# Performance work log

Hardware: AMD Instinct MI355X
Metric: run time of the kernel (lower is better)

Reference implementation:

```python
import jax, jax.numpy as jnp
import numpy as np

B, M, S, D, Q, H = 8, 8192, 128, 512, 32, 8
HD = D // H
LN_EPS = 1e-5


def setup_inputs() -> dict:
    key = jax.random.key(0)
    ks = jax.random.split(key, 12)
    inp = {
        "memory": jax.random.normal(ks[0], (B, M, D), dtype=jnp.float32),
        "context": jax.random.normal(ks[1], (B, S, D), dtype=jnp.float32),
        "memory_mask": jax.random.randint(ks[2], (B, M), 0, 2).astype(bool),
        # learned parameters
        "queries_param": jax.random.normal(ks[3], (Q, D), dtype=jnp.float32) * 0.02,
        "ctx_w": jax.random.normal(ks[4], (D, D), dtype=jnp.float32) / np.sqrt(D),
        "ctx_b": jnp.zeros((D,), dtype=jnp.float32),
        "in_w": jax.random.normal(ks[5], (3 * D, D), dtype=jnp.float32) / np.sqrt(D),
        "in_b": jnp.zeros((3 * D,), dtype=jnp.float32),
        "out_w": jax.random.normal(ks[6], (D, D), dtype=jnp.float32) / np.sqrt(D),
        "out_b": jnp.zeros((D,), dtype=jnp.float32),
        "ln_g": jnp.ones((D,), dtype=jnp.float32),
        "ln_b": jnp.zeros((D,), dtype=jnp.float32),
        "gate_w": jax.random.normal(ks[7], (Q, D), dtype=jnp.float32) / np.sqrt(D),
        "gate_b": jnp.zeros((Q,), dtype=jnp.float32),
    }
    return inp


def _forward(memory, context, memory_mask, queries_param, ctx_w, ctx_b,
             in_w, in_b, out_w, out_b, ln_g, ln_b, gate_w, gate_b):
    b = memory.shape[0]
    # pool context over sequence dim (rank-3 path)
    pooled = context.mean(axis=1)  # [B, D]
    # queries + projected context
    queries = queries_param[None, :, :] + (pooled @ ctx_w.T + ctx_b)[:, None, :]  # [B, Q, D]
    # MultiheadAttention in-projection
    wq, wk, wv = in_w[:D], in_w[D:2 * D], in_w[2 * D:]
    bq, bk, bv = in_b[:D], in_b[D:2 * D], in_b[2 * D:]
    qh = (queries @ wq.T + bq).reshape(b, Q, H, HD).transpose(0, 2, 1, 3)   # [B,H,Q,hd]
    kh = (memory @ wk.T + bk).reshape(b, M, H, HD).transpose(0, 2, 1, 3)    # [B,H,M,hd]
    vh = (memory @ wv.T + bv).reshape(b, M, H, HD).transpose(0, 2, 1, 3)    # [B,H,M,hd]
    scale = 1.0 / np.sqrt(HD)
    scores = jnp.einsum('bhqd,bhkd->bhqk', qh * scale, kh)                  # [B,H,Q,M]
    # key_padding_mask: True in memory_mask means valid; invalid -> -inf
    scores = jnp.where(memory_mask[:, None, None, :], scores, -jnp.inf)
    attn = jax.nn.softmax(scores, axis=-1)                                   # [B,H,Q,M]
    ctx_out = jnp.einsum('bhqk,bhkd->bhqd', attn, vh)
    ctx_out = ctx_out.transpose(0, 2, 1, 3).reshape(b, Q, D)
    readouts = ctx_out @ out_w.T + out_b                                     # [B,Q,D]
    attention = attn.mean(axis=1)                                            # [B,Q,M]
    gates = jax.nn.sigmoid(pooled @ gate_w.T + gate_b)                       # [B,Q]
    readouts = readouts * gates[:, :, None]
    mu = readouts.mean(axis=-1, keepdims=True)
    var = readouts.var(axis=-1, keepdims=True)
    readouts_norm = (readouts - mu) * jax.lax.rsqrt(var + LN_EPS) * ln_g + ln_b
    return readouts_norm, attention, gates, queries


def reference(memory, context, memory_mask, queries_param, ctx_w, ctx_b,
              in_w, in_b, out_w, out_b, ln_g, ln_b, gate_w, gate_b):
    return _forward(memory, context, memory_mask, queries_param, ctx_w, ctx_b,
                    in_w, in_b, out_w, out_b, ln_g, ln_b, gate_w, gate_b)
```

## Files before the change

### kernel.cpp

```cpp
#include <hip/hip_runtime.h>
#include <cstdint>

#define BB 8
#define MM 8192
#define SS 128
#define DD 512
#define QQ 32
#define HH 8
#define HDD 64
#define LN_EPS 1e-5f

typedef __bf16 bf16;
typedef __attribute__((ext_vector_type(8))) __bf16 bf16x8;
typedef __attribute__((ext_vector_type(4))) __bf16 bf16x4;
typedef __attribute__((ext_vector_type(4))) float f32x4;

__global__ __launch_bounds__(512) void k_front(const float* __restrict__ ctx,
                                               const float* __restrict__ ctx_w,
                                               const float* __restrict__ ctx_b,
                                               const float* __restrict__ qp,
                                               const float* __restrict__ gate_w,
                                               const float* __restrict__ gate_b,
                                               float* __restrict__ q_out,
                                               float* __restrict__ gates_out) {
    __shared__ float pl[DD];
    int b = blockIdx.x, t = threadIdx.x;
    const float* p = ctx + (size_t)b * SS * DD + t;
    float s = 0.f;
#pragma unroll 8
    for (int i = 0; i < SS; i++) s += p[(size_t)i * DD];
    pl[t] = s * (1.0f / SS);
    __syncthreads();
    const f32x4* wr = (const f32x4*)(ctx_w + (size_t)t * DD);
    const f32x4* pv = (const f32x4*)pl;
    float acc = 0.f;
#pragma unroll 8
    for (int k = 0; k < DD / 4; k++) {
        f32x4 w = wr[k], pp = pv[k];
        acc += w.x * pp.x + w.y * pp.y + w.z * pp.z + w.w * pp.w;
    }
    float proj = acc + ctx_b[t];
#pragma unroll 4
    for (int q = 0; q < QQ; q++)
        q_out[((size_t)b * QQ + q) * DD + t] = qp[q * DD + t] + proj;
    if (t < QQ) {
        const f32x4* gw = (const f32x4*)(gate_w + (size_t)t * DD);
        float ga = 0.f;
#pragma unroll 8
        for (int k = 0; k < DD / 4; k++) {
            f32x4 w = gw[k], pp = pv[k];
            ga += w.x * pp.x + w.y * pp.y + w.z * pp.z + w.w * pp.w;
        }
        gates_out[b * QQ + t] = 1.0f / (1.0f + __expf(-(ga + gate_b[t])));
    }
}

__global__ void k_qh(const float* __restrict__ q_in, const float* __restrict__ in_w,
                     const float* __restrict__ in_b, float* __restrict__ qh) {
    __shared__ float qr[DD];
    int bq = blockIdx.x, t = threadIdx.x;
    qr[t] = q_in[(size_t)bq * DD + t];
    qr[t + 256] = q_in[(size_t)bq * DD + t + 256];
    __syncthreads();
    const f32x4* qv = (const f32x4*)qr;
#pragma unroll
    for (int jj = 0; jj < 2; jj++) {
        int j = t + jj * 256;
        const f32x4* wv = (const f32x4*)(in_w + (size_t)j * DD);
        float acc = 0.f;
#pragma unroll 8
        for (int k = 0; k < DD / 4; k++) {
            f32x4 w = wv[k], p = qv[k];
            acc += w.x * p.x + w.y * p.y + w.z * p.z + w.w * p.w;
        }
        qh[(size_t)bq * DD + j] = 0.125f * (acc + in_b[j]);
    }
}

__global__ void k_cvt(const float* __restrict__ src, bf16* __restrict__ dst, int n4) {
    int i = blockIdx.x * blockDim.x + threadIdx.x;
    if (i >= n4) return;
    f32x4 v = ((const f32x4*)src)[i];
    bf16x4 o;
    o.x = (bf16)v.x; o.y = (bf16)v.y; o.z = (bf16)v.z; o.w = (bf16)v.w;
    ((bf16x4*)dst)[i] = o;
}

__global__ __launch_bounds__(512) void k_gemm_kv(const bf16* __restrict__ A,
                                                 const bf16* __restrict__ Bw,
                                                 const float* __restrict__ in_b,
                                                 bf16* __restrict__ kvK,
                                                 bf16* __restrict__ Vt) {
    __shared__ __align__(16) bf16 sm[2 * 128 * 64];
    bf16* As = sm;
    bf16* Bs = sm + 128 * 64;
    int tid = threadIdx.x;
    int w = tid >> 6, l = tid & 63;
    int bid = blockIdx.x;
    int bn = (bid >> 3) & 7;
    int bm = ((bid >> 6) << 3) | (bid & 7);
    int wm = w >> 1, wn = w & 1;
    const f32x4 vzero = {0.f, 0.f, 0.f, 0.f};
    f32x4 acc[2][4];
#pragma unroll
    for (int i = 0; i < 2; i++)
#pragma unroll
        for (int j = 0; j < 4; j++) acc[i][j] = vzero;

    int lr = l >> 3;
    int gc = (l & 7) ^ lr;
    const bf16* Ag = A + (size_t)(bm * 128) * DD;
    const bf16* Bg = Bw + (size_t)(bn * 128) * DD;
    int lq = l & 15, quad = l >> 4, lx = lq & 7;

    for (int k0 = 0; k0 < DD; k0 += 64) {
        __syncthreads();
#pragma unroll
        for (int i = 0; i < 2; i++) {
            int seg = w * 2 + i;
            const bf16* ga = Ag + (size_t)(seg * 8 + lr) * DD + k0 + gc * 8;
            const bf16* gb = Bg + (size_t)(seg * 8 + lr) * DD + k0 + gc * 8;
            __builtin_amdgcn_global_load_lds((const __attribute__((address_space(1))) void*)ga,
                                             (__attribute__((address_space(3))) void*)(As + seg * 512),
                                             16, 0, 0);
            __builtin_amdgcn_global_load_lds((const __attribute__((address_space(1))) void*)gb,
                                             (__attribute__((address_space(3))) void*)(Bs + seg * 512),
                                             16, 0, 0);
        }
        __syncthreads();
#pragma unroll
        for (int kc = 0; kc < 8; kc += 4) {
            int ch = (quad + kc) ^ lx;
            bf16x8 af[2], bfr[4];
#pragma unroll
            for (int i = 0; i < 2; i++)
                af[i] = *(const bf16x8*)(As + (wm * 32 + i * 16 + lq) * 64 + ch * 8);
#pragma unroll
            for (int j = 0; j < 4; j++)
                bfr[j] = *(const bf16x8*)(Bs + (wn * 64 + j * 16 + lq) * 64 + ch * 8);
#pragma unroll
            for (int i = 0; i < 2; i++)
#pragma unroll
                for (int j = 0; j < 4; j++)
                    acc[i][j] = __builtin_amdgcn_mfma_f32_16x16x32_bf16(af[i], bfr[j], acc[i][j], 0, 0, 0);
        }
    }

    __syncthreads();
    bf16* tile = sm;
    if (bn < 4) {
#pragma unroll
        for (int j = 0; j < 4; j++) {
            int col = wn * 64 + j * 16 + lq;
            float bias = in_b[512 + bn * 128 + col];
            int cc = col >> 3, cl = col & 7;
#pragma unroll
            for (int i = 0; i < 2; i++) {
                int rbase = wm * 32 + i * 16 + quad * 4;
#pragma unroll
                for (int t = 0; t < 4; t++) {
                    int row = rbase + t;
                    tile[row * 128 + ((cc ^ (row & 15)) << 3) + cl] = (bf16)(acc[i][j][t] + bias);
                }
            }
        }
        __syncthreads();
        for (int idx = tid; idx < 2048; idx += 512) {
            int row = idx >> 4, ch2 = idx & 15;
            bf16x8 v = *(const bf16x8*)(tile + row * 128 + ((ch2 ^ (row & 15)) << 3));
            *(bf16x8*)(kvK + (size_t)(bm * 128 + row) * 512 + bn * 128 + ch2 * 8) = v;
        }
    } else {
#pragma unroll
        for (int j = 0; j < 4; j++) {
            int col = wn * 64 + j * 16 + lq;
            float bias = in_b[512 + bn * 128 + col];
            int cs = col & 15;
#pragma unroll
            for (int i = 0; i < 2; i++) {
                int rbase = wm * 32 + i * 16 + quad * 4;
#pragma unroll
                for (int t = 0; t < 4; t++) {
                    int row = rbase + t;
                    tile[col * 128 + (((row >> 3) ^ cs) << 3) + (row & 7)] = (bf16)(acc[i][j][t] + bias);
                }
            }
        }
        __syncthreads();
        int b = bm >> 6;
        int m0 = (bm & 63) * 128;
        int hd0 = (bn - 4) * 128;
        for (int idx = tid; idx < 2048; idx += 512) {
            int col = idx >> 4, ch2 = idx & 15;
            bf16x8 v = *(const bf16x8*)(tile + col * 128 + ((ch2 ^ (col & 15)) << 3));
            *(bf16x8*)(Vt + ((size_t)(b * 512 + hd0 + col)) * MM + m0 + ch2 * 8) = v;
        }
    }
}

__global__ __launch_bounds__(256) void k_scores(const float* __restrict__ qh,
                                                const bf16* __restrict__ kvK,
                                                const int* __restrict__ mask,
                                                float* __restrict__ scores) {
    int blk = blockIdx.x;
    int mt = blk & 15, h = (blk >> 4) & 7, b = blk >> 7;
    int tid = threadIdx.x, w = tid >> 6, l = tid & 63;
    int lq = l & 15, quad = l >> 4;
    int mbase = mt * 512 + w * 128;

    bf16x8 af[2][2];
#pragma unroll
    for (int i = 0; i < 2; i++)
#pragma unroll
        for (int s = 0; s < 2; s++) {
            const float* qp = qh + ((size_t)(b * QQ + i * 16 + lq)) * DD + h * 64 + s * 32 + quad * 8;
            f32x4 q0 = *(const f32x4*)qp;
            f32x4 q1 = *(const f32x4*)(qp + 4);
            bf16x8 v;
            v[0] = (bf16)q0.x; v[1] = (bf16)q0.y; v[2] = (bf16)q0.z; v[3] = (bf16)q0.w;
            v[4] = (bf16)q1.x; v[5] = (bf16)q1.y; v[6] = (bf16)q1.z; v[7] = (bf16)q1.w;
            af[i][s] = v;
        }

    const f32x4 vzero = {0.f, 0.f, 0.f, 0.f};
    f32x4 acc[2][8];
#pragma unroll
    for (int i = 0; i < 2; i++)
#pragma unroll
        for (int n = 0; n < 8; n++) acc[i][n] = vzero;

#pragma unroll
    for (int n = 0; n < 8; n++) {
        int m = mbase + n * 16 + lq;
        const bf16* kp = kvK + ((size_t)(b * MM + m)) * 512 + h * 64 + quad * 8;
        bf16x8 b0 = *(const bf16x8*)kp;
        bf16x8 b1 = *(const bf16x8*)(kp + 32);
#pragma unroll
        for (int i = 0; i < 2; i++) {
            acc[i][n] = __builtin_amdgcn_mfma_f32_16x16x32_bf16(af[i][0], b0, acc[i][n], 0, 0, 0);
            acc[i][n] = __builtin_amdgcn_mfma_f32_16x16x32_bf16(af[i][1], b1, acc[i][n], 0, 0, 0);
        }
    }
#pragma unroll
    for (int n = 0; n < 8; n++) {
        int m = mbase + n * 16 + lq;
        int mv = mask[b * MM + m];
        float ninf = -__builtin_inff();
#pragma unroll
        for (int i = 0; i < 2; i++)
#pragma unroll
            for (int t = 0; t < 4; t++) {
                int q = i * 16 + quad * 4 + t;
                float val = mv ? acc[i][n][t] : ninf;
                scores[((size_t)(b * HH + h) * QQ + q) * MM + m] = val;
            }
    }
}

__global__ __launch_bounds__(1024) void k_softmax(float* __restrict__ scores,
                                                  float* __restrict__ attn_out) {
    __shared__ float sred[16];
    int bq = blockIdx.x;
    int b = bq >> 5, q = bq & 31;
    int t = threadIdx.x, wid = t >> 6;
    float am[8];
#pragma unroll
    for (int i = 0; i < 8; i++) am[i] = 0.f;

    for (int h = 0; h < HH; h++) {
        float* row = scores + ((size_t)(b * HH + h) * QQ + q) * MM;
        bf16* prow = (bf16*)row;
        float x[8];
#pragma unroll
        for (int i = 0; i < 8; i++) x[i] = row[t + i * 1024];
        float mx = -__builtin_inff();
#pragma unroll
        for (int i = 0; i < 8; i++) mx = fmaxf(mx, x[i]);
        for (int off = 32; off; off >>= 1) mx = fmaxf(mx, __shfl_xor(mx, off, 64));
        if ((t & 63) == 0) sred[wid] = mx;
        __syncthreads();
#pragma unroll
        for (int i = 0; i < 16; i++) mx = fmaxf(mx, sred[i]);
        __syncthreads();
        float sum = 0.f;
#pragma unroll
        for (int i = 0; i < 8; i++) {
            x[i] = __expf(x[i] - mx);
            sum += x[i];
        }
        for (int off = 32; off; off >>= 1) sum += __shfl_xor(sum, off, 64);
        if ((t & 63) == 0) sred[wid] = sum;
        __syncthreads();
        float tot = 0.f;
#pragma unroll
        for (int i = 0; i < 16; i++) tot += sred[i];
        float inv = 1.0f / tot;
#pragma unroll
        for (int i = 0; i < 8; i++) {
            float p = x[i] * inv;
            prow[t + i * 1024] = (bf16)p;
            am[i] += p;
        }
        __syncthreads();
    }
    float* ao = attn_out + (size_t)bq * MM;
#pragma unroll
    for (int i = 0; i < 8; i++) ao[t + i * 1024] = am[i] * (1.0f / HH);
}

__global__ __launch_bounds__(256) void k_pv(const bf16* __restrict__ Pb,
                                            const bf16* __restrict__ Vt,
                                            float* __restrict__ ctxo_p) {
    __shared__ float ctile[QQ * HDD];
    int blk = blockIdx.x;
    int ck = blk & 7, h = (blk >> 3) & 7, b = blk >> 6;
    int t = threadIdx.x, w = t >> 6, l = t & 63;
    int lq = l & 15, quad = l >> 4;
    int m0 = ck * 1024 + w * 256;

    const bf16* Prow0 = Pb + ((size_t)((b * HH + h) * QQ + lq)) * 16384 + m0 + quad * 8;
    const bf16* Prow1 = Prow0 + (size_t)16 * 16384;
    const bf16* Vrow = Vt + ((size_t)((b * HH + h) * HDD + lq)) * MM + m0 + quad * 8;

    const f32x4 vzero = {0.f, 0.f, 0.f, 0.f};
    f32x4 acc[2][4];
#pragma unroll
    for (int i = 0; i < 2; i++)
#pragma unroll
        for (int j = 0; j < 4; j++) acc[i][j] = vzero;

#pragma unroll 2
    for (int ks = 0; ks < 256; ks += 32) {
        bf16x8 a0 = *(const bf16x8*)(Prow0 + ks);
        bf16x8 a1 = *(const bf16x8*)(Prow1 + ks);
        bf16x8 bv[4];
#pragma unroll
        for (int j = 0; j < 4; j++) bv[j] = *(const bf16x8*)(Vrow + (size_t)j * 16 * MM + ks);
#pragma unroll
        for (int j = 0; j < 4; j++) {
            acc[0][j] = __builtin_amdgcn_mfma_f32_16x16x32_bf16(a0, bv[j], acc[0][j], 0, 0, 0);
            acc[1][j] = __builtin_amdgcn_mfma_f32_16x16x32_bf16(a1, bv[j], acc[1][j], 0, 0, 0);
        }
    }
    for (int i = t; i < QQ * HDD; i += 256) ctile[i] = 0.f;
    __syncthreads();
#pragma unroll
    for (int i = 0; i < 2; i++)
#pragma unroll
        for (int j = 0; j < 4; j++)
#pragma unroll
            for (int tt = 0; tt < 4; tt++) {
                int q = i * 16 + quad * 4 + tt;
                int d = j * 16 + lq;
                atomicAdd(&ctile[q * HDD + d], acc[i][j][tt]);
            }
    __syncthreads();
    float* dst = ctxo_p + (size_t)ck * (BB * QQ * DD);
    for (int i = t; i < QQ * HDD; i += 256) {
        int q = i >> 6, d = i & 63;
        dst[((size_t)(b * QQ + q)) * DD + h * HDD + d] = ctile[i];
    }
}

__global__ __launch_bounds__(256) void k_outln(const float* __restrict__ ctxo_p,
                                               const float* __restrict__ out_w,
                                               const float* __restrict__ out_b,
                                               const float* __restrict__ gates,
                                               const float* __restrict__ ln_g,
                                               const float* __restrict__ ln_b,
                                               float* __restrict__ out0) {
    __shared__ float cr[DD];
    __shared__ float sred[4], sred2[4];
    int bq = blockIdx.x, t = threadIdx.x;
    float c0 = 0.f, c1 = 0.f;
#pragma unroll
    for (int c = 0; c < 8; c++) {
        const float* src = ctxo_p + (size_t)c * (BB * QQ * DD) + (size_t)bq * DD;
        c0 += src[t];
        c1 += src[t + 256];
    }
    cr[t] = c0;
    cr[t + 256] = c1;
    __syncthreads();
    float g = gates[bq];
    const f32x4* cv = (const f32x4*)cr;
    float r[2];
#pragma unroll
    for (int jj = 0; jj < 2; jj++) {
        int j = t + jj * 256;
        const f32x4* wv = (const f32x4*)(out_w + (size_t)j * DD);
        float acc = 0.f;
#pragma unroll 4
        for (int k = 0; k < DD / 4; k++) {
            f32x4 wq = wv[k], cq = cv[k];
            acc += wq.x * cq.x + wq.y * cq.y + wq.z * cq.z + wq.w * cq.w;
        }
        r[jj] = (acc + out_b[j]) * g;
    }
    float s1 = r[0] + r[1];
    float s2 = r[0] * r[0] + r[1] * r[1];
    for (int off = 32; off; off >>= 1) {
        s1 += __shfl_xor(s1, off, 64);
        s2 += __shfl_xor(s2, off, 64);
    }
    int wid = t >> 6;
    if ((t & 63) == 0) { sred[wid] = s1; sred2[wid] = s2; }
    __syncthreads();
    float S1 = sred[0] + sred[1] + sred[2] + sred[3];
    float S2 = sred2[0] + sred2[1] + sred2[2] + sred2[3];
    float mu = S1 * (1.0f / DD);
    float var = S2 * (1.0f / DD) - mu * mu;
    float rs = rsqrtf(var + LN_EPS);
#pragma unroll
    for (int jj = 0; jj < 2; jj++) {
        int j = t + jj * 256;
        out0[(size_t)bq * DD + j] = (r[jj] - mu) * rs * ln_g[j] + ln_b[j];
    }
}

extern "C" void kernel_launch(void* const* d_in, const int* in_sizes, int n_in,
                              void* d_out, int out_size, void* d_ws, size_t ws_size,
                              hipStream_t stream) {
    const float* memory  = (const float*)d_in[0];
    const float* context = (const float*)d_in[1];
    const int*   mask    = (const int*)d_in[2];
    const float* qp      = (const float*)d_in[3];
    const float* ctx_w   = (const float*)d_in[4];
    const float* ctx_b   = (const float*)d_in[5];
    const float* in_w    = (const float*)d_in[6];
    const float* in_b    = (const float*)d_in[7];
    const float* out_w   = (const float*)d_in[8];
    const float* out_b   = (const float*)d_in[9];
    const float* ln_g    = (const float*)d_in[10];
    const float* ln_b    = (const float*)d_in[11];
    const float* gate_w  = (const float*)d_in[12];
    const float* gate_b  = (const float*)d_in[13];

    float* out       = (float*)d_out;
    float* out_ln    = out;
    float* out_attn  = out + 131072;
    float* out_gates = out + 131072 + 2097152;
    float* out_q     = out_gates + 256;

    char* ws = (char*)d_ws;
    bf16*  memB   = (bf16*)ws;
    float* scores = (float*)ws;
    bf16*  Pb     = (bf16*)ws;
    bf16*  kvK    = (bf16*)(ws + 67108864);
    bf16*  Vt     = (bf16*)(ws + 134217728);
    bf16*  kvwB   = (bf16*)(ws + 201326592);
    float* qh     = (float*)(ws + 202375168);
    float* ctxo_p = (float*)(ws + 202899456);

    k_front<<<BB, 512, 0, stream>>>(context, ctx_w, ctx_b, qp, gate_w, gate_b, out_q, out_gates);
    k_qh<<<BB * QQ, 256, 0, stream>>>(out_q, in_w, in_b, qh);
    k_cvt<<<32768, 256, 0, stream>>>(memory, memB, 8388608);
    k_cvt<<<512, 256, 0, stream>>>(in_w + 262144, kvwB, 131072);
    k_gemm_kv<<<4096, 512, 0, stream>>>(memB, kvwB, in_b, kvK, Vt);
    k_scores<<<1024, 256, 0, stream>>>(qh, kvK, mask, scores);
    k_softmax<<<BB * QQ, 1024, 0, stream>>>(scores, out_attn);
    k_pv<<<BB * HH * 8, 256, 0, stream>>>(Pb, Vt, ctxo_p);
    k_outln<<<BB * QQ, 256, 0, stream>>>(ctxo_p, out_w, out_b, out_gates, ln_g, ln_b, out_ln);
}
```

Before: 507.1 us.

## Fuse per-chunk softmax stats into scores kernel, store fp16 scores

The scores kernel now computes per-chunk row max and exp-sum, stages scores through shared memory and writes them as fp16 with coalesced stores. This replaces the separate full-row softmax kernel, which read fp32 scores and wrote bf16 probabilities. A new attention-mean kernel and the PV kernel each merge the chunk stats and recompute exp on the fly. This halves score traffic and removes a pass, at the cost of fp16 precision on raw scores and repeated exp work. The q-projection kernel is also reorganised so each weight row is reused across 8 queries.

```diff
diff --git a/kernel.cpp b/kernel.cpp
--- a/kernel.cpp
+++ b/kernel.cpp
@@ -11,9 +11,13 @@
 #define LN_EPS 1e-5f
 
 typedef __bf16 bf16;
+typedef _Float16 f16;
 typedef __attribute__((ext_vector_type(8))) __bf16 bf16x8;
 typedef __attribute__((ext_vector_type(4))) __bf16 bf16x4;
+typedef __attribute__((ext_vector_type(8))) _Float16 f16x8;
 typedef __attribute__((ext_vector_type(4))) float f32x4;
+
+#define NEG_INF (-__builtin_inff())
 
 __global__ __launch_bounds__(512) void k_front(const float* __restrict__ ctx,
                                                const float* __restrict__ ctx_w,
@@ -55,25 +59,37 @@
     }
 }
 
-__global__ void k_qh(const float* __restrict__ q_in, const float* __restrict__ in_w,
-                     const float* __restrict__ in_b, float* __restrict__ qh) {
-    __shared__ float qr[DD];
-    int bq = blockIdx.x, t = threadIdx.x;
-    qr[t] = q_in[(size_t)bq * DD + t];
-    qr[t + 256] = q_in[(size_t)bq * DD + t + 256];
-    __syncthreads();
-    const f32x4* qv = (const f32x4*)qr;
-#pragma unroll
-    for (int jj = 0; jj < 2; jj++) {
-        int j = t + jj * 256;
-        const f32x4* wv = (const f32x4*)(in_w + (size_t)j * DD);
-        float acc = 0.f;
-#pragma unroll 8
-        for (int k = 0; k < DD / 4; k++) {
-            f32x4 w = wv[k], p = qv[k];
-            acc += w.x * p.x + w.y * p.y + w.z * p.z + w.w * p.w;
-        }
-        qh[(size_t)bq * DD + j] = 0.125f * (acc + in_b[j]);
+__global__ __launch_bounds__(256) void k_qh(const float* __restrict__ q_in,
+                                            const float* __restrict__ in_w,
+                                            const float* __restrict__ in_b,
+                                            float* __restrict__ qh) {
+    __shared__ float qr[QQ * DD];
+    int blk = blockIdx.x;
+    int b = blk >> 3, js = blk & 7;
+    int t = threadIdx.x;
+    const f32x4* src = (const f32x4*)(q_in + (size_t)b * QQ * DD);
+    f32x4* dst = (f32x4*)qr;
+    for (int i = t; i < QQ * DD / 4; i += 256) dst[i] = src[i];
+    __syncthreads();
+    int j = js * 64 + (t & 63);
+    int qg = t >> 6;
+    const f32x4* wv = (const f32x4*)(in_w + (size_t)j * DD);
+    float acc[8];
+#pragma unroll
+    for (int e = 0; e < 8; e++) acc[e] = 0.f;
+    for (int k = 0; k < DD / 4; k++) {
+        f32x4 w = wv[k];
+#pragma unroll
+        for (int e = 0; e < 8; e++) {
+            f32x4 qq = ((const f32x4*)qr)[(qg * 8 + e) * (DD / 4) + k];
+            acc[e] += w.x * qq.x + w.y * qq.y + w.z * qq.z + w.w * qq.w;
+        }
+    }
+    float bias = in_b[j];
+#pragma unroll
+    for (int e = 0; e < 8; e++) {
+        int q = qg * 8 + e;
+        qh[((size_t)(b * QQ + q)) * DD + j] = 0.125f * (acc[e] + bias);
     }
 }
 
@@ -201,7 +217,13 @@
 __global__ __launch_bounds__(256) void k_scores(const float* __restrict__ qh,
                                                 const bf16* __restrict__ kvK,
                                                 const int* __restrict__ mask,
-                                                float* __restrict__ scores) {
+                                                f16* __restrict__ s16,
+                                                float* __restrict__ statsM,
+                                                float* __restrict__ statsS) {
+    __shared__ __align__(16) f16 tile[QQ * 528];
+    __shared__ float smx[QQ][4];
+    __shared__ float sse[QQ][4];
+    __shared__ float qmax[QQ];
     int blk = blockIdx.x;
     int mt = blk & 15, h = (blk >> 4) & 7, b = blk >> 7;
     int tid = threadIdx.x, w = tid >> 6, l = tid & 63;
@@ -243,84 +265,158 @@
     }
 #pragma unroll
     for (int n = 0; n < 8; n++) {
-        int m = mbase + n * 16 + lq;
-        int mv = mask[b * MM + m];
-        float ninf = -__builtin_inff();
+        int mv = mask[b * MM + mbase + n * 16 + lq];
+        if (!mv) {
+#pragma unroll
+            for (int i = 0; i < 2; i++)
+#pragma unroll
+                for (int t = 0; t < 4; t++) acc[i][n][t] = NEG_INF;
+        }
+    }
+    float mx[2][4];
+#pragma unroll
+    for (int i = 0; i < 2; i++)
+#pragma unroll
+        for (int t = 0; t < 4; t++) {
+            float m = acc[i][0][t];
+#pragma unroll
+            for (int n = 1; n < 8; n++) m = fmaxf(m, acc[i][n][t]);
+            mx[i][t] = m;
+        }
+#pragma unroll
+    for (int off = 1; off < 16; off <<= 1)
 #pragma unroll
         for (int i = 0; i < 2; i++)
 #pragma unroll
-            for (int t = 0; t < 4; t++) {
-                int q = i * 16 + quad * 4 + t;
-                float val = mv ? acc[i][n][t] : ninf;
-                scores[((size_t)(b * HH + h) * QQ + q) * MM + m] = val;
-            }
-    }
-}
-
-__global__ __launch_bounds__(1024) void k_softmax(float* __restrict__ scores,
-                                                  float* __restrict__ attn_out) {
-    __shared__ float sred[16];
-    int bq = blockIdx.x;
-    int b = bq >> 5, q = bq & 31;
-    int t = threadIdx.x, wid = t >> 6;
+            for (int t = 0; t < 4; t++) mx[i][t] = fmaxf(mx[i][t], __shfl_xor(mx[i][t], off, 64));
+    if (lq == 0) {
+#pragma unroll
+        for (int i = 0; i < 2; i++)
+#pragma unroll
+            for (int t = 0; t < 4; t++) smx[i * 16 + quad * 4 + t][w] = mx[i][t];
+    }
+    __syncthreads();
+    if (tid < QQ) qmax[tid] = fmaxf(fmaxf(smx[tid][0], smx[tid][1]), fmaxf(smx[tid][2], smx[tid][3]));
+    __syncthreads();
+    float se[2][4];
+#pragma unroll
+    for (int i = 0; i < 2; i++)
+#pragma unroll
+        for (int t = 0; t < 4; t++) {
+            float qm = qmax[i * 16 + quad * 4 + t];
+            float s = 0.f;
+#pragma unroll
+            for (int n = 0; n < 8; n++) s += __expf(acc[i][n][t] - qm);
+            se[i][t] = s;
+        }
+#pragma unroll
+    for (int off = 1; off < 16; off <<= 1)
+#pragma unroll
+        for (int i = 0; i < 2; i++)
+#pragma unroll
+            for (int t = 0; t < 4; t++) se[i][t] += __shfl_xor(se[i][t], off, 64);
+    if (lq == 0) {
+#pragma unroll
+        for (int i = 0; i < 2; i++)
+#pragma unroll
+            for (int t = 0; t < 4; t++) sse[i * 16 + quad * 4 + t][w] = se[i][t];
+    }
+#pragma unroll
+    for (int n = 0; n < 8; n++) {
+        int mloc = w * 128 + n * 16 + lq;
+#pragma unroll
+        for (int i = 0; i < 2; i++)
+#pragma unroll
+            for (int t = 0; t < 4; t++)
+                tile[(i * 16 + quad * 4 + t) * 528 + mloc] = (f16)acc[i][n][t];
+    }
+    __syncthreads();
+    if (tid < QQ) {
+        statsM[(size_t)blk * QQ + tid] = qmax[tid];
+        statsS[(size_t)blk * QQ + tid] = sse[tid][0] + sse[tid][1] + sse[tid][2] + sse[tid][3];
+    }
+    for (int it = tid; it < 2048; it += 256) {
+        int q = it >> 6, c = it & 63;
+        f16x8 v = *(const f16x8*)(tile + q * 528 + c * 8);
+        *(f16x8*)(s16 + ((size_t)((b * HH + h) * QQ + q)) * MM + mt * 512 + c * 8) = v;
+    }
+}
+
+__global__ __launch_bounds__(256) void k_attn(const f16* __restrict__ s16,
+                                              const float* __restrict__ statsM,
+                                              const float* __restrict__ statsS,
+                                              float* __restrict__ attn_out) {
+    __shared__ float cM[128], cS[128], Mh[HH], iLh[HH];
+    int blk = blockIdx.x;
+    int ms = blk & 3, q = (blk >> 2) & 31, b = blk >> 7;
+    int t = threadIdx.x;
+    if (t < 128) {
+        int h = t >> 4, c = t & 15;
+        size_t sidx = (size_t)(((b * HH + h) * 16 + c)) * QQ + q;
+        cM[t] = statsM[sidx];
+        cS[t] = statsS[sidx];
+    }
+    __syncthreads();
+    if (t < HH) {
+        float M = NEG_INF;
+#pragma unroll
+        for (int c = 0; c < 16; c++) M = fmaxf(M, cM[t * 16 + c]);
+        float L = 0.f;
+#pragma unroll
+        for (int c = 0; c < 16; c++) L += cS[t * 16 + c] * __expf(cM[t * 16 + c] - M);
+        Mh[t] = M;
+        iLh[t] = (1.0f / L) * (1.0f / HH);
+    }
+    __syncthreads();
+    int m0 = ms * 2048 + t * 8;
     float am[8];
 #pragma unroll
-    for (int i = 0; i < 8; i++) am[i] = 0.f;
-
+    for (int e = 0; e < 8; e++) am[e] = 0.f;
+#pragma unroll
     for (int h = 0; h < HH; h++) {
-        float* row = scores + ((size_t)(b * HH + h) * QQ + q) * MM;
-        bf16* prow = (bf16*)row;
-        float x[8];
-#pragma unroll
-        for (int i = 0; i < 8; i++) x[i] = row[t + i * 1024];
-        float mx = -__builtin_inff();
-#pragma unroll
-        for (int i = 0; i < 8; i++) mx = fmaxf(mx, x[i]);
-        for (int off = 32; off; off >>= 1) mx = fmaxf(mx, __shfl_xor(mx, off, 64));
-        if ((t & 63) == 0) sred[wid] = mx;
-        __syncthreads();
-#pragma unroll
-        for (int i = 0; i < 16; i++) mx = fmaxf(mx, sred[i]);
-        __syncthreads();
-        float sum = 0.f;
-#pragma unroll
-        for (int i = 0; i < 8; i++) {
-            x[i] = __expf(x[i] - mx);
-            sum += x[i];
-        }
-        for (int off = 32; off; off >>= 1) sum += __shfl_xor(sum, off, 64);
-        if ((t & 63) == 0) sred[wid] = sum;
-        __syncthreads();
-        float tot = 0.f;
-#pragma unroll
-        for (int i = 0; i < 16; i++) tot += sred[i];
-        float inv = 1.0f / tot;
-#pragma unroll
-        for (int i = 0; i < 8; i++) {
-            float p = x[i] * inv;
-            prow[t + i * 1024] = (bf16)p;
-            am[i] += p;
-        }
-        __syncthreads();
-    }
-    float* ao = attn_out + (size_t)bq * MM;
-#pragma unroll
-    for (int i = 0; i < 8; i++) ao[t + i * 1024] = am[i] * (1.0f / HH);
-}
-
-__global__ __launch_bounds__(256) void k_pv(const bf16* __restrict__ Pb,
+        f16x8 v = *(const f16x8*)(s16 + ((size_t)((b * HH + h) * QQ + q)) * MM + m0);
+        float M = Mh[h], iL = iLh[h];
+#pragma unroll
+        for (int e = 0; e < 8; e++) am[e] += __expf((float)v[e] - M) * iL;
+    }
+    float* ao = attn_out + (size_t)(b * QQ + q) * MM + m0;
+    f32x4 o0 = {am[0], am[1], am[2], am[3]};
+    f32x4 o1 = {am[4], am[5], am[6], am[7]};
+    *(f32x4*)ao = o0;
+    *(f32x4*)(ao + 4) = o1;
+}
+
+__global__ __launch_bounds__(256) void k_pv(const f16* __restrict__ s16,
+                                            const float* __restrict__ statsM,
+                                            const float* __restrict__ statsS,
                                             const bf16* __restrict__ Vt,
                                             float* __restrict__ ctxo_p) {
     __shared__ float ctile[QQ * HDD];
+    __shared__ float Mq[QQ], iLq[QQ];
     int blk = blockIdx.x;
     int ck = blk & 7, h = (blk >> 3) & 7, b = blk >> 6;
     int t = threadIdx.x, w = t >> 6, l = t & 63;
     int lq = l & 15, quad = l >> 4;
+    if (t < QQ) {
+        const float* pM = statsM + (size_t)((b * HH + h) * 16) * QQ + t;
+        const float* pS = statsS + (size_t)((b * HH + h) * 16) * QQ + t;
+        float M = NEG_INF;
+#pragma unroll
+        for (int c = 0; c < 16; c++) M = fmaxf(M, pM[c * QQ]);
+        float L = 0.f;
+#pragma unroll
+        for (int c = 0; c < 16; c++) L += pS[c * QQ] * __expf(pM[c * QQ] - M);
+        Mq[t] = M;
+        iLq[t] = 1.0f / L;
+    }
+    __syncthreads();
     int m0 = ck * 1024 + w * 256;
 
-    const bf16* Prow0 = Pb + ((size_t)((b * HH + h) * QQ + lq)) * 16384 + m0 + quad * 8;
-    const bf16* Prow1 = Prow0 + (size_t)16 * 16384;
+    const f16* P0 = s16 + ((size_t)((b * HH + h) * QQ + lq)) * MM + m0 + quad * 8;
+    const f16* P1 = P0 + (size_t)16 * MM;
     const bf16* Vrow = Vt + ((size_t)((b * HH + h) * HDD + lq)) * MM + m0 + quad * 8;
+    float M0 = Mq[lq], iL0 = iLq[lq];
+    float M1 = Mq[16 + lq], iL1 = iLq[16 + lq];
 
     const f32x4 vzero = {0.f, 0.f, 0.f, 0.f};
     f32x4 acc[2][4];
@@ -331,8 +427,13 @@
 
 #pragma unroll 2
     for (int ks = 0; ks < 256; ks += 32) {
-        bf16x8 a0 = *(const bf16x8*)(Prow0 + ks);
-        bf16x8 a1 = *(const bf16x8*)(Prow1 + ks);
+        f16x8 r0 = *(const f16x8*)(P0 + ks);
+        f16x8 r1 = *(const f16x8*)(P1 + ks);
+        bf16x8 a0, a1;
+#pragma unroll
+        for (int e = 0; e < 8; e++) a0[e] = (bf16)(__expf((float)r0[e] - M0) * iL0);
+#pragma unroll
+        for (int e = 0; e < 8; e++) a1[e] = (bf16)(__expf((float)r1[e] - M1) * iL1);
         bf16x8 bv[4];
 #pragma unroll
         for (int j = 0; j < 4; j++) bv[j] = *(const bf16x8*)(Vrow + (size_t)j * 16 * MM + ks);
@@ -444,21 +545,22 @@
 
     char* ws = (char*)d_ws;
     bf16*  memB   = (bf16*)ws;
-    float* scores = (float*)ws;
-    bf16*  Pb     = (bf16*)ws;
+    f16*   s16    = (f16*)ws;
     bf16*  kvK    = (bf16*)(ws + 67108864);
     bf16*  Vt     = (bf16*)(ws + 134217728);
     bf16*  kvwB   = (bf16*)(ws + 201326592);
+    float* statsM = (float*)(ws + 201588736);
+    float* statsS = (float*)(ws + 201719808);
     float* qh     = (float*)(ws + 202375168);
     float* ctxo_p = (float*)(ws + 202899456);
 
     k_front<<<BB, 512, 0, stream>>>(context, ctx_w, ctx_b, qp, gate_w, gate_b, out_q, out_gates);
-    k_qh<<<BB * QQ, 256, 0, stream>>>(out_q, in_w, in_b, qh);
+    k_qh<<<64, 256, 0, stream>>>(out_q, in_w, in_b, qh);
     k_cvt<<<32768, 256, 0, stream>>>(memory, memB, 8388608);
     k_cvt<<<512, 256, 0, stream>>>(in_w + 262144, kvwB, 131072);
     k_gemm_kv<<<4096, 512, 0, stream>>>(memB, kvwB, in_b, kvK, Vt);
-    k_scores<<<1024, 256, 0, stream>>>(qh, kvK, mask, scores);
-    k_softmax<<<BB * QQ, 1024, 0, stream>>>(scores, out_attn);
-    k_pv<<<BB * HH * 8, 256, 0, stream>>>(Pb, Vt, ctxo_p);
+    k_scores<<<1024, 256, 0, stream>>>(qh, kvK, mask, s16, statsM, statsS);
+    k_attn<<<1024, 256, 0, stream>>>(s16, statsM, statsS, out_attn);
+    k_pv<<<512, 256, 0, stream>>>(s16, statsM, statsS, Vt, ctxo_p);
     k_outln<<<BB * QQ, 256, 0, stream>>>(ctxo_p, out_w, out_b, out_gates, ln_g, ln_b, out_ln);
 }
```

Result: faster. 484.2 us (-4.5%).
